# Optimization experiments

Measured on AMD Instinct MI355X. Metric: run time of the kernel, lower is better.

The kernel has to match this reference:

```python
import jax, jax.numpy as jnp
import numpy as np

EPS = 1e-12  # torch f.normalize eps


def _rms_norm(x, g):
    # f.normalize(x, dim=1) * g * sqrt(C): L2-normalize over channel dim
    c = x.shape[1]
    n = jnp.maximum(jnp.linalg.norm(x, axis=1, keepdims=True), EPS)
    return x / n * g * (c ** 0.5)


def setup_inputs() -> dict:
    key = jax.random.key(0)
    ks = jax.random.split(key, 5)
    b, dim, H, W = 32, 256, 64, 64
    heads, dim_head, num_mem = 4, 32, 4
    hidden = heads * dim_head
    return {
        "x": jax.random.normal(ks[0], (b, dim, H, W), dtype=jnp.float32),
        "g1": jnp.ones((1, dim, 1, 1), dtype=jnp.float32),
        "mem_kv": jax.random.normal(ks[1], (2, heads, dim_head, num_mem), dtype=jnp.float32),
        "w_qkv": jax.random.normal(ks[2], (3 * hidden, dim), dtype=jnp.float32) * (1.0 / np.sqrt(dim)),
        "w_out": jax.random.normal(ks[3], (dim, hidden), dtype=jnp.float32) * (1.0 / np.sqrt(hidden)),
        "b_out": jnp.zeros((dim,), dtype=jnp.float32),
        "g2": jnp.ones((1, dim, 1, 1), dtype=jnp.float32),
    }


def reference(x, g1, mem_kv, w_qkv, w_out, b_out, g2):
    b, c, H, W = x.shape
    _, heads, dim_head, num_mem = mem_kv.shape
    n = H * W
    scale = dim_head ** -0.5

    xn = _rms_norm(x, g1)
    # 1x1 conv qkv projection: [b, 3*hidden, H, W]
    qkv = jnp.einsum('oc,bchw->bohw', w_qkv, xn)
    hidden = heads * dim_head
    q, k, v = jnp.split(qkv, 3, axis=1)
    # b (h d) x y -> b h d (x y)
    q = q.reshape(b, heads, dim_head, n)
    k = k.reshape(b, heads, dim_head, n)
    v = v.reshape(b, heads, dim_head, n)

    mk = jnp.broadcast_to(mem_kv[0], (b, heads, dim_head, num_mem))
    mv = jnp.broadcast_to(mem_kv[1], (b, heads, dim_head, num_mem))
    k = jnp.concatenate([mk, k], axis=-1)
    v = jnp.concatenate([mv, v], axis=-1)

    q = jax.nn.softmax(q, axis=-2) * scale  # softmax over head dim d
    k = jax.nn.softmax(k, axis=-1)          # softmax over sequence n

    context = jnp.einsum('bhdn,bhen->bhde', k, v)   # [b,h,d,e]
    out = jnp.einsum('bhde,bhdn->bhen', context, q)  # [b,h,e,n]
    out = out.reshape(b, hidden, H, W)

    o = jnp.einsum('oc,bchw->bohw', w_out, out) + b_out[None, :, None, None]
    return _rms_norm(o, g2)
```

## Files before the change

### kernel.cpp

```cpp
#include <hip/hip_runtime.h>
#include <math.h>

#define CC   256
#define HW   4096
#define OC3  384
#define HID  128
#define DH   32
#define NM   4
#define NPART 8
#define SCALE 0.17677669529663688f

typedef __bf16 bf16x8 __attribute__((ext_vector_type(8)));
typedef float  f32x4  __attribute__((ext_vector_type(4)));

__device__ __forceinline__ ushort f2bf(float x) {
    union { float f; unsigned u; } v; v.f = x;
    unsigned r = v.u + 0x7fffu + ((v.u >> 16) & 1u);
    return (ushort)(r >> 16);
}
__device__ __forceinline__ float bf2f(ushort b) {
    union { unsigned u; float f; } v; v.u = ((unsigned)b) << 16; return v.f;
}
__device__ __forceinline__ void g2l16(const void* g, void* l) {
    __builtin_amdgcn_global_load_lds(
        (const __attribute__((address_space(1))) void*)g,
        (__attribute__((address_space(3))) void*)l, 16, 0, 0);
}

__global__ __launch_bounds__(256) void k_xn(const float* __restrict__ x,
        const float* __restrict__ wqkv, const float* __restrict__ g1,
        const float* __restrict__ wout,
        ushort* __restrict__ wq2t, ushort* __restrict__ woutt,
        ushort* __restrict__ xnT) {
    __shared__ float xt[256 * 36];
    __shared__ float ps[8 * 33];
    __shared__ float invn[32];
    int tid = threadIdx.x;
    if (blockIdx.x < 384) {
        int o = blockIdx.x;
        wq2t[(size_t)o * CC + tid] = f2bf(wqkv[(size_t)o * CC + tid] * g1[tid] * 16.0f);
        if (o < CC && tid < HID) woutt[(size_t)o * HID + tid] = f2bf(wout[(size_t)o * HID + tid]);
    }
    int pix0 = blockIdx.x * 32;
    int b = pix0 >> 12, hw0 = pix0 & 4095;
    int p = tid & 31, cg = tid >> 5;
    const float* xb = x + (size_t)b * CC * HW + hw0;
    {
        int cr = tid >> 3;
        int chunk = tid & 7;
        #pragma unroll
        for (int pass = 0; pass < 8; ++pass) {
            int c = pass * 32 + cr;
            float4 v = *(const float4*)&xb[(size_t)c * HW + chunk * 4];
            *(float4*)&xt[c * 36 + chunk * 4] = v;
        }
    }
    __syncthreads();
    float s = 0.f;
    #pragma unroll 8
    for (int i = 0; i < 32; ++i) { float v = xt[(cg * 32 + i) * 36 + p]; s += v * v; }
    ps[cg * 33 + p] = s;
    __syncthreads();
    if (tid < 32) {
        float t = 0.f;
        #pragma unroll
        for (int g = 0; g < 8; ++g) t += ps[g * 33 + tid];
        invn[tid] = 1.0f / fmaxf(sqrtf(t), 1e-12f);
    }
    __syncthreads();
    float inv = invn[p];
    ushort* dst = xnT + ((size_t)(pix0 + p)) * CC + cg * 32;
    #pragma unroll
    for (int q = 0; q < 4; ++q) {
        uint4 pk; ushort* o8 = (ushort*)&pk;
        #pragma unroll
        for (int i = 0; i < 8; ++i) o8[i] = f2bf(xt[(cg * 32 + q * 8 + i) * 36 + p] * inv);
        *(uint4*)&dst[q * 8] = pk;
    }
}

__global__ __launch_bounds__(256) void k_qkv(const ushort* __restrict__ wq2t,
        const ushort* __restrict__ xnT, ushort* __restrict__ qkv) {
    __shared__ __align__(16) ushort As[2][128 * 32];
    __shared__ __align__(16) ushort Bs[2][128 * 32];
    int tid = threadIdx.x;
    int lin = blockIdx.x + 3 * (blockIdx.y + 32 * blockIdx.z);
    int swz = (lin & 7) * 384 + (lin >> 3);
    int m0 = (swz % 3) * 128;
    int t_ = swz / 3;
    int p0 = (t_ & 31) * 128;
    int b  = t_ >> 5;
    int lane = tid & 63, wid = tid >> 6;
    int l15 = tid & 15, quad = (tid >> 4) & 3;
    int wm = wid >> 1, wn = wid & 1;
    int rsub = lane >> 2;
    const ushort* Ab = wq2t + (size_t)m0 * CC;
    const ushort* Bb = xnT + ((size_t)(b * HW + p0)) * CC;
    f32x4 acc[4][4];
    #pragma unroll
    for (int i = 0; i < 4; ++i)
        #pragma unroll
        for (int j = 0; j < 4; ++j) acc[i][j] = (f32x4){0.f, 0.f, 0.f, 0.f};

    auto stage = [&](int buf, int k0) {
        #pragma unroll
        for (int q = 0; q < 2; ++q) {
            int rw = wid * 32 + q * 16;
            int r  = rw + rsub;
            int sc = (lane & 3) ^ ((r >> 1) & 3);
            g2l16(Ab + (size_t)r * CC + k0 + sc * 8, &As[buf][rw * 32]);
            g2l16(Bb + (size_t)r * CC + k0 + sc * 8, &Bs[buf][rw * 32]);
        }
    };

    stage(0, 0);
    __syncthreads();
    #pragma unroll
    for (int s = 0; s < 8; ++s) {
        int cur = s & 1;
        if (s < 7) stage(cur ^ 1, (s + 1) * 32);
        bf16x8 af[4], bfr[4];
        #pragma unroll
        for (int mt = 0; mt < 4; ++mt) {
            int ra = wm * 64 + mt * 16 + l15;
            af[mt] = *(const bf16x8*)&As[cur][ra * 32 + ((quad ^ ((ra >> 1) & 3)) << 3)];
        }
        #pragma unroll
        for (int nt = 0; nt < 4; ++nt) {
            int rb = wn * 64 + nt * 16 + l15;
            bfr[nt] = *(const bf16x8*)&Bs[cur][rb * 32 + ((quad ^ ((rb >> 1) & 3)) << 3)];
        }
        #pragma unroll
        for (int mt = 0; mt < 4; ++mt)
            #pragma unroll
            for (int nt = 0; nt < 4; ++nt)
                acc[mt][nt] = __builtin_amdgcn_mfma_f32_16x16x32_bf16(
                                  af[mt], bfr[nt], acc[mt][nt], 0, 0, 0);
        __syncthreads();
    }
    #pragma unroll
    for (int mt = 0; mt < 4; ++mt) {
        int o = m0 + wm * 64 + mt * 16 + quad * 4;
        #pragma unroll
        for (int nt = 0; nt < 4; ++nt) {
            int pix = p0 + wn * 64 + nt * 16 + l15;
            ushort* dst = qkv + ((size_t)(b * OC3 + o)) * HW + pix;
            #pragma unroll
            for (int r = 0; r < 4; ++r) dst[(size_t)r * HW] = f2bf(acc[mt][nt][r]);
        }
    }
}

__global__ void k_ksoft(const ushort* __restrict__ qkv, const float* __restrict__ memkv,
                        float* __restrict__ kmaxb, float* __restrict__ rsumb) {
    int row = blockIdx.x * 4 + (threadIdx.x >> 6);
    int lane = threadIdx.x & 63;
    int b = row >> 7, hd = row & 127;
    const ushort* kp = qkv + ((size_t)(b * OC3 + HID + hd)) * HW;
    uint4 kreg[8];
    #pragma unroll
    for (int i = 0; i < 8; ++i) kreg[i] = *(const uint4*)&kp[i * 512 + lane * 8];
    float m = -1e30f;
    #pragma unroll
    for (int i = 0; i < 8; ++i) {
        const ushort* e = (const ushort*)&kreg[i];
        #pragma unroll
        for (int j = 0; j < 8; ++j) m = fmaxf(m, bf2f(e[j]));
    }
    #pragma unroll
    for (int s = 1; s < 64; s <<= 1) m = fmaxf(m, __shfl_xor(m, s));
    const float* mk = memkv + hd * NM;
    #pragma unroll
    for (int j = 0; j < NM; ++j) m = fmaxf(m, mk[j]);
    float s = 0.f;
    #pragma unroll
    for (int i = 0; i < 8; ++i) {
        const ushort* e = (const ushort*)&kreg[i];
        #pragma unroll
        for (int j = 0; j < 8; ++j) s += __expf(bf2f(e[j]) - m);
    }
    #pragma unroll
    for (int t = 1; t < 64; t <<= 1) s += __shfl_xor(s, t);
    #pragma unroll
    for (int j = 0; j < NM; ++j) s += __expf(mk[j] - m);
    if (lane == 0) { kmaxb[row] = m; rsumb[row] = 1.0f / s; }
}

__global__ __launch_bounds__(256) void k_ctx(const ushort* __restrict__ qkv,
        const float* __restrict__ memkv, const float* __restrict__ kmaxb,
        const float* __restrict__ rsumb, float* __restrict__ ctxp) {
    __shared__ __align__(16) char smem[32768];
    ushort* klw = (ushort*)smem;
    ushort* vlw = (ushort*)(smem + 16384);
    float*  red = (float*)smem;
    int tid = threadIdx.x;
    int lane = tid & 63, wid = tid >> 6;
    int l15 = lane & 15, quad = lane >> 4;
    int bh = blockIdx.x, part = blockIdx.y;
    int b = bh >> 2, h = bh & 3;
    int rowbase = bh * DH;
    int r  = lane >> 1;
    int ch = (lane & 1) * 32;
    const ushort* kp = qkv + ((size_t)(b * OC3 + HID + h * DH) + r) * HW + part * 512;
    const ushort* vp = qkv + ((size_t)(b * OC3 + 2 * HID + h * DH) + r) * HW + part * 512;
    float kmr = kmaxb[rowbase + r], rsr = rsumb[rowbase + r];
    ushort* myk = klw + wid * 2048;
    ushort* myv = vlw + wid * 2048;
    f32x4 acc[2][2];
    #pragma unroll
    for (int i = 0; i < 2; ++i)
        #pragma unroll
        for (int j = 0; j < 2; ++j) acc[i][j] = (f32x4){0.f, 0.f, 0.f, 0.f};

    #pragma unroll
    for (int t = 0; t < 2; ++t) {
        int n0 = wid * 64 + t * 256;
        #pragma unroll
        for (int i = 0; i < 4; ++i) {
            uint4 kv4 = *(const uint4*)&kp[n0 + ch + i * 8];
            uint4 vv4 = *(const uint4*)&vp[n0 + ch + i * 8];
            uint4 ko; ushort* kw = (ushort*)&ko; const ushort* ke = (const ushort*)&kv4;
            #pragma unroll
            for (int j = 0; j < 8; ++j) kw[j] = f2bf(__expf(bf2f(ke[j]) - kmr) * rsr);
            int boff = ((ch + i * 8) * 2) ^ ((r & 7) << 4);
            *(uint4*)((char*)&myk[r * 64] + boff) = ko;
            *(uint4*)((char*)&myv[r * 64] + boff) = vv4;
        }
        #pragma unroll
        for (int ks = 0; ks < 2; ++ks) {
            bf16x8 af[2], bf[2];
            #pragma unroll
            for (int dt = 0; dt < 2; ++dt) {
                int row = dt * 16 + l15;
                int boff = (ks * 64 + quad * 16) ^ ((row & 7) << 4);
                af[dt] = *(const bf16x8*)((char*)&myk[row * 64] + boff);
                bf[dt] = *(const bf16x8*)((char*)&myv[row * 64] + boff);
            }
            #pragma unroll
            for (int dt = 0; dt < 2; ++dt)
                #pragma unroll
                for (int et = 0; et < 2; ++et)
                    acc[dt][et] = __builtin_amdgcn_mfma_f32_16x16x32_bf16(
                                      af[dt], bf[et], acc[dt][et], 0, 0, 0);
        }
    }
    __syncthreads();
    #pragma unroll
    for (int dt = 0; dt < 2; ++dt)
        #pragma unroll
        for (int et = 0; et < 2; ++et)
            #pragma unroll
            for (int rr = 0; rr < 4; ++rr) {
                int d = dt * 16 + quad * 4 + rr;
                int e = et * 16 + l15;
                red[wid * 1024 + d * 32 + e] = acc[dt][et][rr];
            }
    __syncthreads();
    {
        int o0 = tid * 4;
        f32x4 s4 = (f32x4){0.f, 0.f, 0.f, 0.f};
        #pragma unroll
        for (int w = 0; w < 4; ++w) {
            f32x4 v = *(const f32x4*)&red[w * 1024 + o0];
            s4[0] += v[0]; s4[1] += v[1]; s4[2] += v[2]; s4[3] += v[3];
        }
        if (part == 0) {
            int d = o0 >> 5;
            float km = kmaxb[rowbase + d], rsm = rsumb[rowbase + d];
            #pragma unroll
            for (int q = 0; q < 4; ++q) {
                int e = (o0 + q) & 31;
                #pragma unroll
                for (int m = 0; m < NM; ++m) {
                    float kw = __expf(memkv[(h * DH + d) * NM + m] - km) * rsm;
                    s4[q] += kw * memkv[512 + (h * DH + e) * NM + m];
                }
            }
        }
        *(f32x4*)&ctxp[(size_t)part * 131072 + (size_t)bh * 1024 + o0] = s4;
    }
}

__global__ __launch_bounds__(256) void k_w2(const float* __restrict__ ctxp,
        const ushort* __restrict__ woutt, ushort* __restrict__ W2) {
    __shared__ ushort ctxb[4 * 32 * 40];
    int tid = threadIdx.x, b = blockIdx.x;
    int wid = tid >> 6;
    int l15 = tid & 15, quad = (tid >> 4) & 3;
    #pragma unroll
    for (int j = 0; j < 16; ++j) {
        int idx = tid + j * 256;
        float s = 0.f;
        #pragma unroll
        for (int p = 0; p < NPART; ++p)
            s += ctxp[(size_t)p * 131072 + (size_t)b * 4096 + idx];
        int h = idx >> 10, d = (idx >> 5) & 31, e = idx & 31;
        ctxb[(h * 32 + d) * 40 + e] = f2bf(s);
    }
    __syncthreads();
    #pragma unroll
    for (int h = 0; h < 4; ++h) {
        f32x4 acc[4][2];
        #pragma unroll
        for (int i = 0; i < 4; ++i)
            #pragma unroll
            for (int j = 0; j < 2; ++j) acc[i][j] = (f32x4){0.f, 0.f, 0.f, 0.f};
        bf16x8 af[4], bfr[2];
        #pragma unroll
        for (int mt = 0; mt < 4; ++mt)
            af[mt] = *(const bf16x8*)&woutt[(size_t)(wid * 64 + mt * 16 + l15) * HID
                                            + h * DH + quad * 8];
        #pragma unroll
        for (int nt = 0; nt < 2; ++nt)
            bfr[nt] = *(const bf16x8*)&ctxb[(h * 32 + nt * 16 + l15) * 40 + quad * 8];
        #pragma unroll
        for (int mt = 0; mt < 4; ++mt)
            #pragma unroll
            for (int nt = 0; nt < 2; ++nt)
                acc[mt][nt] = __builtin_amdgcn_mfma_f32_16x16x32_bf16(
                                  af[mt], bfr[nt], acc[mt][nt], 0, 0, 0);
        #pragma unroll
        for (int mt = 0; mt < 4; ++mt)
            #pragma unroll
            for (int nt = 0; nt < 2; ++nt)
                #pragma unroll
                for (int r = 0; r < 4; ++r) {
                    int oc = wid * 64 + mt * 16 + quad * 4 + r;
                    int d  = nt * 16 + l15;
                    W2[((size_t)b * CC + oc) * HID + h * DH + d] = f2bf(acc[mt][nt][r]);
                }
    }
}

__global__ __launch_bounds__(256) void k_final(const ushort* __restrict__ qkv,
        const ushort* __restrict__ W2, const float* __restrict__ bout,
        const float* __restrict__ g2, float* __restrict__ y) {
    __shared__ __align__(16) ushort sq[64 * 136];
    __shared__ __align__(16) ushort WsQ[256 * 32];
    __shared__ float red[64 * 17];
    __shared__ float invs[64];
    __shared__ float bl[256];
    __shared__ float gl[256];
    int tid = threadIdx.x;
    int b = blockIdx.y;
    int hwb = blockIdx.x * 64;
    int lane = tid & 63, wid = tid >> 6;
    int l15 = tid & 15, quad = (tid >> 4) & 3;
    bl[tid] = bout[tid];
    gl[tid] = g2[tid];

    {
        const ushort* qb = qkv + ((size_t)b * OC3) * HW + hwb;
        #pragma unroll
        for (int pass = 0; pass < 4; ++pass) {
            int r0 = pass * 32 + wid * 8;
            int row = r0 + (lane >> 3);
            g2l16(qb + (size_t)row * HW + (lane & 7) * 8, &WsQ[r0 * 64]);
        }
    }
    __syncthreads();

    {
        float vd[32];
        float m = -1e30f;
        #pragma unroll
        for (int d = 0; d < 32; ++d) {
            float v = bf2f(WsQ[(wid * 32 + d) * 64 + lane]);
            vd[d] = v; m = fmaxf(m, v);
        }
        float s = 0.f;
        #pragma unroll
        for (int d = 0; d < 32; ++d) { float e = __expf(vd[d] - m); vd[d] = e; s += e; }
        float r_ = SCALE / s;
        #pragma unroll
        for (int q8 = 0; q8 < 4; ++q8) {
            uint4 pk; ushort* o8 = (ushort*)&pk;
            #pragma unroll
            for (int i = 0; i < 8; ++i) o8[i] = f2bf(vd[q8 * 8 + i] * r_);
            *(uint4*)&sq[lane * 136 + wid * DH + q8 * 8] = pk;
        }
    }

    f32x4 acc[4][4];
    #pragma unroll
    for (int i = 0; i < 4; ++i)
        #pragma unroll
        for (int j = 0; j < 4; ++j) acc[i][j] = (f32x4){0.f, 0.f, 0.f, 0.f};
    int rsub = lane >> 2;
    const ushort* W2b = W2 + (size_t)b * CC * HID;
    for (int k0 = 0; k0 < HID; k0 += 32) {
        __syncthreads();
        #pragma unroll
        for (int q = 0; q < 4; ++q) {
            int rw = wid * 64 + q * 16;
            int r  = rw + rsub;
            int sc = (lane & 3) ^ ((r >> 1) & 3);
            g2l16(W2b + (size_t)r * HID + k0 + sc * 8, &WsQ[rw * 32]);
        }
        __syncthreads();
        bf16x8 af[4], bfr[4];
        #pragma unroll
        for (int mt = 0; mt < 4; ++mt) {
            int ra = wid * 64 + mt * 16 + l15;
            af[mt] = *(const bf16x8*)&WsQ[ra * 32 + ((quad ^ ((ra >> 1) & 3)) << 3)];
        }
        #pragma unroll
        for (int nt = 0; nt < 4; ++nt)
            bfr[nt] = *(const bf16x8*)&sq[(nt * 16 + l15) * 136 + k0 + quad * 8];
        #pragma unroll
        for (int mt = 0; mt < 4; ++mt)
            #pragma unroll
            for (int nt = 0; nt < 4; ++nt)
                acc[mt][nt] = __builtin_amdgcn_mfma_f32_16x16x32_bf16(
                                  af[mt], bfr[nt], acc[mt][nt], 0, 0, 0);
    }

    float part[4] = {0.f, 0.f, 0.f, 0.f};
    #pragma unroll
    for (int mt = 0; mt < 4; ++mt)
        #pragma unroll
        for (int r = 0; r < 4; ++r) {
            int oc = wid * 64 + mt * 16 + quad * 4 + r;
            float bo = bl[oc];
            #pragma unroll
            for (int nt = 0; nt < 4; ++nt) {
                float v = acc[mt][nt][r] + bo;
                acc[mt][nt][r] = v;
                part[nt] += v * v;
            }
        }
    __syncthreads();
    #pragma unroll
    for (int nt = 0; nt < 4; ++nt)
        red[(nt * 16 + l15) * 17 + wid * 4 + quad] = part[nt];
    __syncthreads();
    if (tid < 64) {
        float s = 0.f;
        #pragma unroll
        for (int g = 0; g < 16; ++g) s += red[tid * 17 + g];
        invs[tid] = 1.0f / fmaxf(sqrtf(s), 1e-12f);
    }
    __syncthreads();
    #pragma unroll
    for (int mt = 0; mt < 4; ++mt)
        #pragma unroll
        for (int nt = 0; nt < 4; ++nt) {
            int pix = nt * 16 + l15;
            float iv = invs[pix];
            #pragma unroll
            for (int r = 0; r < 4; ++r) {
                int oc = wid * 64 + mt * 16 + quad * 4 + r;
                y[((size_t)(b * CC + oc)) * HW + hwb + pix] = acc[mt][nt][r] * iv * gl[oc] * 16.0f;
            }
        }
}

extern "C" void kernel_launch(void* const* d_in, const int* in_sizes, int n_in,
                              void* d_out, int out_size, void* d_ws, size_t ws_size,
                              hipStream_t stream) {
    const float* x     = (const float*)d_in[0];
    const float* g1    = (const float*)d_in[1];
    const float* memkv = (const float*)d_in[2];
    const float* wqkv  = (const float*)d_in[3];
    const float* wout  = (const float*)d_in[4];
    const float* bout  = (const float*)d_in[5];
    const float* g2    = (const float*)d_in[6];
    float* y = (float*)d_out;

    char* w = (char*)d_ws;
    ushort* wq2t  = (ushort*)w;  w += (size_t)OC3 * CC * 2;
    ushort* woutt = (ushort*)w;  w += (size_t)CC * HID * 2;
    float*  kmaxb = (float*)w;   w += 4096 * 4;
    float*  rsumb = (float*)w;   w += 4096 * 4;
    float*  ctxp  = (float*)w;   w += (size_t)NPART * 131072 * 4;
    ushort* W2    = (ushort*)w;  w += (size_t)32 * CC * HID * 2;
    ushort* xnT   = (ushort*)w;  w += (size_t)32 * HW * CC * 2;
    ushort* qkv   = (ushort*)w;  w += (size_t)32 * OC3 * HW * 2;

    k_xn    <<<dim3(4096),      dim3(256), 0, stream>>>(x, wqkv, g1, wout, wq2t, woutt, xnT);
    k_qkv   <<<dim3(3, 32, 32), dim3(256), 0, stream>>>(wq2t, xnT, qkv);
    k_ksoft <<<dim3(1024),      dim3(256), 0, stream>>>(qkv, memkv, kmaxb, rsumb);
    k_ctx   <<<dim3(128, 8),    dim3(256), 0, stream>>>(qkv, memkv, kmaxb, rsumb, ctxp);
    k_w2    <<<dim3(32),        dim3(256), 0, stream>>>(ctxp, woutt, W2);
    k_final <<<dim3(64, 32),    dim3(256), 0, stream>>>(qkv, W2, bout, g2, y);
}
```

Measured before the change: 353.9 us.

## Fuse Q projection into final kernel, skip writing Q to global

The qkv GEMM now computes only the K and V rows (grid shrinks from 3 to 2 M-tiles). The final kernel recomputes the Q projection for its 64-pixel tile from xnT and the Q weights with MFMA, applies the head-dim softmax directly in registers, and feeds the result into the output projection. This removes the Q round-trip through HBM, a third of the qkv write traffic. In exchange the final kernel does extra GEMM work, uses more shared memory, and runs a more complex staging pipeline.

```diff
diff --git a/kernel.cpp b/kernel.cpp
--- a/kernel.cpp
+++ b/kernel.cpp
@@ -84,10 +84,10 @@
     __shared__ __align__(16) ushort As[2][128 * 32];
     __shared__ __align__(16) ushort Bs[2][128 * 32];
     int tid = threadIdx.x;
-    int lin = blockIdx.x + 3 * (blockIdx.y + 32 * blockIdx.z);
-    int swz = (lin & 7) * 384 + (lin >> 3);
-    int m0 = (swz % 3) * 128;
-    int t_ = swz / 3;
+    int lin = blockIdx.x + 2 * (blockIdx.y + 32 * blockIdx.z);
+    int swz = (lin & 7) * 256 + (lin >> 3);
+    int m0 = 128 + (swz % 2) * 128;
+    int t_ = swz / 2;
     int p0 = (t_ & 31) * 128;
     int b  = t_ >> 5;
     int lane = tid & 63, wid = tid >> 6;
@@ -332,61 +332,117 @@
     }
 }
 
-__global__ __launch_bounds__(256) void k_final(const ushort* __restrict__ qkv,
-        const ushort* __restrict__ W2, const float* __restrict__ bout,
-        const float* __restrict__ g2, float* __restrict__ y) {
-    __shared__ __align__(16) ushort sq[64 * 136];
-    __shared__ __align__(16) ushort WsQ[256 * 32];
-    __shared__ float red[64 * 17];
-    __shared__ float invs[64];
-    __shared__ float bl[256];
-    __shared__ float gl[256];
+__global__ __launch_bounds__(256) void k_final(const ushort* __restrict__ xnT,
+        const ushort* __restrict__ wq2t, const ushort* __restrict__ W2,
+        const float* __restrict__ bout, const float* __restrict__ g2,
+        float* __restrict__ y) {
+    __shared__ __align__(16) char smem[52224];
+    ushort* xnTs = (ushort*)smem;
+    float*  red  = (float*)smem;
+    float*  invs = (float*)(smem + 4352);
+    ushort* Qw   = (ushort*)(smem + 16384);
+    ushort* sq   = (ushort*)(smem + 32768);
+    float*  bl   = (float*)(smem + 50176);
+    float*  gl   = (float*)(smem + 51200);
     int tid = threadIdx.x;
     int b = blockIdx.y;
     int hwb = blockIdx.x * 64;
     int lane = tid & 63, wid = tid >> 6;
     int l15 = tid & 15, quad = (tid >> 4) & 3;
+    int rsub = lane >> 2;
     bl[tid] = bout[tid];
     gl[tid] = g2[tid];
 
-    {
-        const ushort* qb = qkv + ((size_t)b * OC3) * HW + hwb;
-        #pragma unroll
-        for (int pass = 0; pass < 4; ++pass) {
-            int r0 = pass * 32 + wid * 8;
-            int row = r0 + (lane >> 3);
-            g2l16(qb + (size_t)row * HW + (lane & 7) * 8, &WsQ[r0 * 64]);
-        }
-    }
-    __syncthreads();
-
-    {
-        float vd[32];
+    auto stageX = [&](int half) {
+        const ushort* xb = xnT + ((size_t)(b * HW + hwb)) * CC + half * 128;
+        #pragma unroll
+        for (int qq = 0; qq < 4; ++qq) {
+            int r0 = qq * 16 + wid * 4;
+            int r  = r0 + (lane >> 4);
+            int g  = (lane & 15) ^ (r & 7);
+            g2l16(xb + (size_t)r * CC + g * 8, &xnTs[r0 * 128]);
+        }
+    };
+    auto stageQ = [&](int buf, int k0) {
+        #pragma unroll
+        for (int qq = 0; qq < 2; ++qq) {
+            int rw = wid * 32 + qq * 16;
+            int r  = rw + rsub;
+            int sc = (lane & 3) ^ ((r >> 1) & 3);
+            g2l16(wq2t + (size_t)r * CC + k0 + sc * 8, &Qw[buf * 4096 + rw * 32]);
+        }
+    };
+
+    f32x4 accq[2][4];
+    #pragma unroll
+    for (int i = 0; i < 2; ++i)
+        #pragma unroll
+        for (int j = 0; j < 4; ++j) accq[i][j] = (f32x4){0.f, 0.f, 0.f, 0.f};
+    stageX(0);
+    stageQ(0, 0);
+    __syncthreads();
+    #pragma unroll
+    for (int s = 0; s < 8; ++s) {
+        int cur = s & 1;
+        if (s < 7 && s != 3) stageQ(cur ^ 1, (s + 1) * 32);
+        bf16x8 af[2], bfr[4];
+        #pragma unroll
+        for (int mt = 0; mt < 2; ++mt) {
+            int ra = wid * 32 + mt * 16 + l15;
+            af[mt] = *(const bf16x8*)&Qw[cur * 4096 + ra * 32 + ((quad ^ ((ra >> 1) & 3)) << 3)];
+        }
+        int cread = (s & 3) * 4 + quad;
+        #pragma unroll
+        for (int nt = 0; nt < 4; ++nt) {
+            int rb = nt * 16 + l15;
+            bfr[nt] = *(const bf16x8*)&xnTs[rb * 128 + ((cread ^ (rb & 7)) << 3)];
+        }
+        #pragma unroll
+        for (int mt = 0; mt < 2; ++mt)
+            #pragma unroll
+            for (int nt = 0; nt < 4; ++nt)
+                accq[mt][nt] = __builtin_amdgcn_mfma_f32_16x16x32_bf16(
+                                   af[mt], bfr[nt], accq[mt][nt], 0, 0, 0);
+        if (s == 3) {
+            __syncthreads();
+            stageX(1);
+            stageQ(cur ^ 1, 128);
+        }
+        __syncthreads();
+    }
+
+    #pragma unroll
+    for (int nt = 0; nt < 4; ++nt) {
         float m = -1e30f;
         #pragma unroll
-        for (int d = 0; d < 32; ++d) {
-            float v = bf2f(WsQ[(wid * 32 + d) * 64 + lane]);
-            vd[d] = v; m = fmaxf(m, v);
-        }
+        for (int mt = 0; mt < 2; ++mt)
+            #pragma unroll
+            for (int r = 0; r < 4; ++r) m = fmaxf(m, accq[mt][nt][r]);
+        m = fmaxf(m, __shfl_xor(m, 16));
+        m = fmaxf(m, __shfl_xor(m, 32));
         float s = 0.f;
-        #pragma unroll
-        for (int d = 0; d < 32; ++d) { float e = __expf(vd[d] - m); vd[d] = e; s += e; }
+        float e[2][4];
+        #pragma unroll
+        for (int mt = 0; mt < 2; ++mt)
+            #pragma unroll
+            for (int r = 0; r < 4; ++r) { e[mt][r] = __expf(accq[mt][nt][r] - m); s += e[mt][r]; }
+        s += __shfl_xor(s, 16);
+        s += __shfl_xor(s, 32);
         float r_ = SCALE / s;
-        #pragma unroll
-        for (int q8 = 0; q8 < 4; ++q8) {
-            uint4 pk; ushort* o8 = (ushort*)&pk;
-            #pragma unroll
-            for (int i = 0; i < 8; ++i) o8[i] = f2bf(vd[q8 * 8 + i] * r_);
-            *(uint4*)&sq[lane * 136 + wid * DH + q8 * 8] = pk;
-        }
-    }
-
+        int pix = nt * 16 + l15;
+        #pragma unroll
+        for (int mt = 0; mt < 2; ++mt)
+            #pragma unroll
+            for (int r = 0; r < 4; ++r)
+                sq[pix * 136 + wid * 32 + mt * 16 + quad * 4 + r] = f2bf(e[mt][r] * r_);
+    }
+
+    ushort* WsQ = Qw;
     f32x4 acc[4][4];
     #pragma unroll
     for (int i = 0; i < 4; ++i)
         #pragma unroll
         for (int j = 0; j < 4; ++j) acc[i][j] = (f32x4){0.f, 0.f, 0.f, 0.f};
-    int rsub = lane >> 2;
     const ushort* W2b = W2 + (size_t)b * CC * HID;
     for (int k0 = 0; k0 < HID; k0 += 32) {
         __syncthreads();
@@ -478,9 +534,9 @@
     ushort* qkv   = (ushort*)w;  w += (size_t)32 * OC3 * HW * 2;
 
     k_xn    <<<dim3(4096),      dim3(256), 0, stream>>>(x, wqkv, g1, wout, wq2t, woutt, xnT);
-    k_qkv   <<<dim3(3, 32, 32), dim3(256), 0, stream>>>(wq2t, xnT, qkv);
+    k_qkv   <<<dim3(2, 32, 32), dim3(256), 0, stream>>>(wq2t, xnT, qkv);
     k_ksoft <<<dim3(1024),      dim3(256), 0, stream>>>(qkv, memkv, kmaxb, rsumb);
     k_ctx   <<<dim3(128, 8),    dim3(256), 0, stream>>>(qkv, memkv, kmaxb, rsumb, ctxp);
     k_w2    <<<dim3(32),        dim3(256), 0, stream>>>(ctxp, woutt, W2);
-    k_final <<<dim3(64, 32),    dim3(256), 0, stream>>>(qkv, W2, bout, g2, y);
-}
+    k_final <<<dim3(64, 32),    dim3(256), 0, stream>>>(xnT, wq2t, W2, bout, g2, y);
+}
```

Result: no change. 353.4 us (-0.1%).
